# Kernel tuning notes

Measured on AMD Instinct MI355X. Metric: run time of the kernel, lower is better.

Reference implementation:

```python
import jax, jax.numpy as jnp
import numpy as np

B, C, H, W = 2, 64, 256, 256
K, DG, PAD = 3, 8, 1
KK = K * K
CG = C // DG


def _conv(x, w, b):
    y = jax.lax.conv_general_dilated(x, w, (1, 1), [(PAD, PAD), (PAD, PAD)],
                                     dimension_numbers=('NCHW', 'OIHW', 'NCHW'))
    return y + b[None, :, None, None]


def _bilinear_one(img, y, x):
    # img: (CG, H, W); y, x: (KK, H, W) float sampling coords; zero-padded bilinear
    y0 = jnp.floor(y)
    x0 = jnp.floor(x)
    wy = y - y0
    wx = x - x0

    def tap(yi, xi, wgt):
        valid = (yi >= 0) & (yi < H) & (xi >= 0) & (xi < W)
        yc = jnp.clip(yi, 0, H - 1).astype(jnp.int32)
        xc = jnp.clip(xi, 0, W - 1).astype(jnp.int32)
        v = img[:, yc, xc]  # (CG, KK, H, W)
        return v * (wgt * valid)[None]

    return (tap(y0, x0, (1 - wy) * (1 - wx)) +
            tap(y0, x0 + 1, (1 - wy) * wx) +
            tap(y0 + 1, x0, wy * (1 - wx)) +
            tap(y0 + 1, x0 + 1, wy * wx))


_sample = jax.vmap(jax.vmap(_bilinear_one))  # over batch, then deform group


def setup_inputs() -> dict:
    key = jax.random.key(0)
    ks = jax.random.split(key, 7)
    n_off = 2 * KK * DG
    n_msk = KK * DG
    bound = 1.0 / np.sqrt(C * K * K)  # kaiming_uniform(a=sqrt(5)) bound
    return {
        'ref': jax.random.normal(ks[0], (B, C, H, W), jnp.float32),
        'neighbour': jax.random.normal(ks[1], (B, C, H, W), jnp.float32),
        'off_w': jax.random.normal(ks[2], (n_off, 2 * C, K, K), jnp.float32) * 0.01,
        'off_b': jnp.zeros((n_off,), jnp.float32),
        'mask_w': jax.random.normal(ks[3], (n_msk, 2 * C, K, K), jnp.float32) * 0.01,
        'mask_b': jnp.zeros((n_msk,), jnp.float32),
        'weight': jax.random.uniform(ks[4], (C, C, K, K), jnp.float32, -bound, bound),
        'bias': jnp.zeros((C,), jnp.float32),
    }


def reference(ref, neighbour, off_w, off_b, mask_w, mask_b, weight, bias):
    concat = jnp.concatenate([ref, neighbour], axis=1)            # (B, 2C, H, W)
    offset = _conv(concat, off_w, off_b)                          # (B, 2*DG*KK, H, W)
    mask = jax.nn.sigmoid(_conv(concat, mask_w, mask_b))          # (B, DG*KK, H, W)

    off = offset.reshape(B, DG, KK, 2, H, W)
    dy, dx = off[:, :, :, 0], off[:, :, :, 1]

    ki, kj = jnp.meshgrid(jnp.arange(K), jnp.arange(K), indexing='ij')
    ki = ki.reshape(KK).astype(jnp.float32)
    kj = kj.reshape(KK).astype(jnp.float32)
    base_y = jnp.arange(H, dtype=jnp.float32)[None, :, None] - PAD + ki[:, None, None]
    base_x = jnp.arange(W, dtype=jnp.float32)[None, None, :] - PAD + kj[:, None, None]
    ys = dy + base_y                                              # (B, DG, KK, H, W)
    xs = dx + base_x

    img_g = neighbour.reshape(B, DG, CG, H, W)
    sampled = _sample(img_g, ys, xs)                              # (B, DG, CG, KK, H, W)
    sampled = sampled * mask.reshape(B, DG, 1, KK, H, W)

    wr = weight.reshape(C, DG, CG, KK)
    out = jnp.einsum('bgckhw,ogck->bohw', sampled, wr)
    return out + bias[None, :, None, None]
```

## Files before the change

### kernel.cpp

```cpp
#include <hip/hip_runtime.h>
#include <hip/hip_fp16.h>
#include <cstdint>
#include <cstddef>

#define B_ 2
#define C_ 64
#define H_ 256
#define W_ 256
#define HW_ (H_*W_)
#define DG_ 8
#define CG_ 8
#define KK_ 9
#define NOFF_ 144
#define NMSK_ 72
#define NTOT_ 216
#define KRED_ 1152
#define XPH_ 258

typedef __bf16 bf16x8 __attribute__((ext_vector_type(8)));
typedef _Float16 half8 __attribute__((ext_vector_type(8)));
typedef short  short8 __attribute__((ext_vector_type(8)));
typedef float  f32x4  __attribute__((ext_vector_type(4)));

__device__ __forceinline__ short f2bf(float f) {
    union { float f; uint32_t u; } a; a.f = f;
    uint32_t u = a.u;
    uint32_t r = (u + 0x7fffu + ((u >> 16) & 1u)) >> 16;
    return (short)r;
}

typedef __attribute__((address_space(1))) const unsigned int g_u32;
typedef __attribute__((address_space(3))) unsigned int l_u32;
__device__ __forceinline__ void gl_lds16(const void* g, void* l) {
    __builtin_amdgcn_global_load_lds((g_u32*)g, (l_u32*)l, 16, 0, 0);
}

__global__ void wtrans2_kernel(const float* __restrict__ off_w,
                               const float* __restrict__ msk_w,
                               short* __restrict__ Bw) {
    int idx = blockIdx.x * 256 + threadIdx.x;
    int s    = idx >> 13;
    int rem  = idx & 8191;
    int n    = rem >> 5;
    int slot = (rem >> 3) & 3;
    int j    = rem & 7;
    int q    = slot ^ ((n >> 1) & 3);
    int c4   = s / 9;
    int tap  = s - c4 * 9;
    int ch   = c4 * 32 + q * 8 + j;
    float v = 0.f;
    if (n < NOFF_)      v = off_w[(size_t)n * KRED_ + ch * 9 + tap];
    else if (n < NTOT_) v = msk_w[(size_t)(n - NOFF_) * KRED_ + ch * 9 + tap];
    Bw[idx] = f2bf(v);
}

__global__ void wtrans3_kernel(const float* __restrict__ weight,
                               short* __restrict__ Bw3) {
    int idx = blockIdx.x * 256 + threadIdx.x;
    int kc   = idx >> 11;
    int rem  = idx & 2047;
    int n    = rem >> 5;
    int slot = (rem >> 3) & 3;
    int j    = rem & 7;
    int q    = slot ^ ((n >> 1) & 3);
    int k    = kc >> 1;
    int g    = ((kc & 1) << 2) + q;
    int ci   = g * 8 + j;
    union { _Float16 h; short s; } cv;
    cv.h = (_Float16)weight[((size_t)n * 64 + ci) * 9 + k];
    Bw3[idx] = cv.s;
}

__global__ void pack_xp2(const float* __restrict__ ref,
                         const float* __restrict__ nbr,
                         short* __restrict__ xp,
                         short* __restrict__ nbf) {
    const int by = blockIdx.x;
    const int b  = by / XPH_;
    const int yi = by - b * XPH_;
    const int c4 = blockIdx.y;
    const int yg = yi - 1;
    const float* base = (c4 < 2 ? ref : nbr) + ((size_t)b * 64 + (c4 & 1) * 32) * HW_;
    short* rowbase = xp + (((size_t)(b * 4 + c4) * XPH_ + yi) * XPH_) * 32;
    for (int xi = threadIdx.x; xi < XPH_; xi += 256) {
        const int xg = xi - 1;
        const bool valid = ((unsigned)yg < H_) && ((unsigned)xg < W_);
        short* dst = rowbase + (size_t)xi * 32;
        const int sig = (xi >> 1) & 3;
        #pragma unroll
        for (int q = 0; q < 4; ++q) {
            float v[8];
            if (valid) {
                const float* p = base + (size_t)(q * 8) * HW_ + (size_t)yg * W_ + xg;
                #pragma unroll
                for (int j = 0; j < 8; ++j) v[j] = p[(size_t)j * HW_];
            } else {
                #pragma unroll
                for (int j = 0; j < 8; ++j) v[j] = 0.f;
            }
            short8 o;
            #pragma unroll
            for (int j = 0; j < 8; ++j) o[j] = f2bf(v[j]);
            *reinterpret_cast<short8*>(dst + ((q ^ sig) * 8)) = o;
            if (c4 >= 2 && valid) {
                const int g = (c4 - 2) * 4 + q;
                union { half8 h8; short8 s8; } u;
                #pragma unroll
                for (int j = 0; j < 8; ++j) u.h8[j] = (_Float16)v[j];
                *reinterpret_cast<short8*>(
                    nbf + ((size_t)(b * 8 + g) * HW_ + (size_t)yg * W_ + xg) * 8) = u.s8;
            }
        }
    }
}

__global__ __launch_bounds__(512, 4) void conv_mfma(
    const short* __restrict__ xp, const short* __restrict__ Bw,
    const float* __restrict__ off_b, const float* __restrict__ msk_b,
    __half* __restrict__ off_o, __half* __restrict__ msk_o)
{
    __shared__ __align__(16) short As[2][4608];

    const int tid  = threadIdx.x;
    const int lane = tid & 63;
    const int wid  = tid >> 6;
    const int wm   = wid & 1;
    const int wn   = wid >> 1;
    const int col     = lane & 15;
    const int quad    = lane >> 4;
    const int rowbase = quad * 4;

    const int bid = blockIdx.x;
    const int wg  = (bid & 7) * 128 + (bid >> 3);
    const int m0 = wg << 7;
    const int b  = m0 >> 16;
    const int h  = (m0 >> 8) & 255;
    const int w0 = m0 & 255;

    int bOff[4];
    #pragma unroll
    for (int nt = 0; nt < 4; ++nt) {
        int n = wn * 64 + nt * 16 + col;
        bOff[nt] = (n * 4 + (quad ^ ((n >> 1) & 3))) * 8;
    }
    int pxv[4];
    #pragma unroll
    for (int mt = 0; mt < 4; ++mt) pxv[mt] = wm * 64 + mt * 16 + col;

    f32x4 acc[4][4];
    #pragma unroll
    for (int i = 0; i < 4; ++i)
        #pragma unroll
        for (int j = 0; j < 4; ++j) acc[i][j] = f32x4{0.f, 0.f, 0.f, 0.f};

    auto stageA = [&](int win, int bb) {
        const int c4s = win / 3;
        const int dys = win - c4s * 3;
        const short* sA = xp + (((size_t)(b * 4 + c4s) * XPH_ + (h + dys)) * XPH_
                                + w0) * 32;
        char* dA = (char*)&As[bb][0];
        gl_lds16(sA + (size_t)tid * 8, dA + wid * 1024);
        if (tid < 32) gl_lds16(sA + (size_t)(512 + tid) * 8, dA + 8192);
    };

    stageA(0, 0);
    __syncthreads();

    #pragma unroll 1
    for (int win = 0; win < 12; ++win) {
        const int bb = win & 1;
        if (win < 11) stageA(win + 1, bb ^ 1);
        const short* AsC = &As[bb][0];

        #pragma unroll
        for (int dx = 0; dx < 3; ++dx) {
            const int s = win * 3 + dx;
            const short* bp = Bw + ((size_t)s << 13);

            bf16x8 bv[4];
            #pragma unroll
            for (int nt = 0; nt < 4; ++nt)
                bv[nt] = *reinterpret_cast<const bf16x8*>(bp + bOff[nt]);

            bf16x8 af[4];
            #pragma unroll
            for (int mt = 0; mt < 4; ++mt) {
                const int px = pxv[mt] + dx;
                af[mt] = *reinterpret_cast<const bf16x8*>(
                    &AsC[(px * 4 + (quad ^ ((px >> 1) & 3))) * 8]);
            }

            #pragma unroll
            for (int mt = 0; mt < 4; ++mt)
                #pragma unroll
                for (int nt = 0; nt < 4; ++nt)
                    acc[mt][nt] = __builtin_amdgcn_mfma_f32_16x16x32_bf16(
                        af[mt], bv[nt], acc[mt][nt], 0, 0, 0);
        }
        __syncthreads();
    }

    #pragma unroll
    for (int mt = 0; mt < 4; ++mt) {
        const int wloc = w0 + wm * 64 + mt * 16 + rowbase;
        #pragma unroll
        for (int nt = 0; nt < 4; ++nt) {
            const int n = wn * 64 + nt * 16 + col;
            if (n >= NTOT_) continue;
            const bool is_off = (n < NOFF_);
            const float bia = is_off ? off_b[n] : msk_b[n - NOFF_];
            union { uint2 u; __half hx[4]; } pk;
            #pragma unroll
            for (int rr = 0; rr < 4; ++rr) {
                float v = acc[mt][nt][rr] + bia;
                if (!is_off) v = 1.f / (1.f + __expf(-v));
                pk.hx[rr] = __float2half(v);
            }
            __half* dst = is_off
                ? (off_o + ((size_t)(b * NOFF_ + n) * H_ + h) * W_ + wloc)
                : (msk_o + ((size_t)(b * NMSK_ + (n - NOFF_)) * H_ + h) * W_ + wloc);
            *(uint2*)dst = pk.u;
        }
    }
}

struct OffV { float dy, dx, mm; };
struct GathV { half8 c00, c01, c10, c11; float a00, a01, a10, a11; };

__global__ __launch_bounds__(512, 4) void apply_mfma(
    const short* __restrict__ nbf, const __half* __restrict__ off_o,
    const __half* __restrict__ msk_o, const short* __restrict__ Bw3,
    const float* __restrict__ bias, float* __restrict__ out)
{
    __shared__ __align__(16) short As[2][128 * 32];

    const int tid  = threadIdx.x;
    const int lane = tid & 63;
    const int wid  = tid >> 6;
    const int col  = lane & 15;
    const int quad = lane >> 4;
    const int wm   = wid & 1;
    const int wn   = wid >> 1;

    const int bid = blockIdx.x;
    const int wg  = (bid & 7) * 128 + (bid >> 3);
    const int m0  = wg << 7;
    const int b   = m0 >> 16;
    const int h   = (m0 >> 8) & 255;
    const int w0  = m0 & 255;

    const int p     = tid & 127;
    const int q     = tid >> 7;
    const int w     = w0 + p;
    const int pix   = h * W_ + w;
    const int slotW = q ^ ((p >> 1) & 3);

    auto loadOffs = [&](int kc) -> OffV {
        const int k = kc >> 1;
        const int g = ((kc & 1) << 2) + q;
        OffV o;
        o.dy = __half2float(off_o[((size_t)(b * NOFF_ + g * 18 + 2 * k)) * HW_ + pix]);
        o.dx = __half2float(off_o[((size_t)(b * NOFF_ + g * 18 + 2 * k + 1)) * HW_ + pix]);
        o.mm = __half2float(msk_o[((size_t)(b * NMSK_ + g * 9 + k)) * HW_ + pix]);
        return o;
    };

    auto issueGather = [&](int kc, OffV o) -> GathV {
        const int k  = kc >> 1;
        const int g  = ((kc & 1) << 2) + q;
        const int ky = k / 3;
        const int kx = k - ky * 3;
        float ys = (float)(h - 1 + ky) + o.dy;
        float xs = (float)(w - 1 + kx) + o.dx;
        float y0f = floorf(ys), x0f = floorf(xs);
        float wy = ys - y0f, wx = xs - x0f;
        int y0 = (int)y0f, x0 = (int)x0f;
        int y1 = y0 + 1, x1 = x0 + 1;
        int yc0 = min(max(y0, 0), H_-1), yc1 = min(max(y1, 0), H_-1);
        float wy0v = (1.f - wy) * (((unsigned)y0 < H_) ? o.mm : 0.f);
        float wy1v = wy * (((unsigned)y1 < H_) ? o.mm : 0.f);
        int xb = min(max(x0, 0), W_-2);
        float wx0v = (((unsigned)x0 < W_) ? (1.f - wx) : 0.f);
        float wx1v = (((unsigned)x1 < W_) ? wx : 0.f);
        float sx0 = (x0 == xb) ? wx0v : ((x1 == xb) ? wx1v : 0.f);
        float sx1 = (x1 == xb + 1) ? wx1v : ((x0 == xb + 1) ? wx0v : 0.f);
        GathV gv;
        gv.a00 = wy0v * sx0; gv.a01 = wy0v * sx1;
        gv.a10 = wy1v * sx0; gv.a11 = wy1v * sx1;
        const short* nb = nbf + (size_t)(b * 8 + g) * HW_ * 8;
        const short* r0 = nb + ((size_t)yc0 * W_ + xb) * 8;
        const short* r1 = nb + ((size_t)yc1 * W_ + xb) * 8;
        gv.c00 = *reinterpret_cast<const half8*>(r0);
        gv.c01 = *reinterpret_cast<const half8*>(r0 + 8);
        gv.c10 = *reinterpret_cast<const half8*>(r1);
        gv.c11 = *reinterpret_cast<const half8*>(r1 + 8);
        return gv;
    };

    auto combineWrite = [&](int kc, const GathV& gv) {
        union { half8 h8; short8 s8; } u;
        #pragma unroll
        for (int c = 0; c < CG_; ++c) {
            float v = gv.a00 * (float)gv.c00[c] + gv.a01 * (float)gv.c01[c]
                    + gv.a10 * (float)gv.c10[c] + gv.a11 * (float)gv.c11[c];
            u.h8[c] = (_Float16)v;
        }
        *reinterpret_cast<short8*>(&As[kc & 1][(p * 4 + slotW) * 8]) = u.s8;
    };

    const int nB = wn * 16 + col;
    const short* bPtr = Bw3 + ((nB * 4 + (quad ^ ((nB >> 1) & 3))) << 3);

    f32x4 acc[4];
    #pragma unroll
    for (int mt = 0; mt < 4; ++mt) acc[mt] = f32x4{0.f, 0.f, 0.f, 0.f};

    {
        OffV o0 = loadOffs(0);
        GathV g0 = issueGather(0, o0);
        combineWrite(0, g0);
    }
    OffV oA = loadOffs(1);
    GathV G = issueGather(1, oA);
    oA = loadOffs(2);
    OffV oB = loadOffs(3);
    __syncthreads();

    #pragma unroll 1
    for (int kc = 0; kc < 18; ++kc) {
        const int bb = kc & 1;
        const short* AsC = &As[bb][0];

        half8 bv = *reinterpret_cast<const half8*>(bPtr + ((size_t)kc << 11));
        half8 af[4];
        #pragma unroll
        for (int mt = 0; mt < 4; ++mt) {
            const int px = wm * 64 + mt * 16 + col;
            af[mt] = *reinterpret_cast<const half8*>(
                &AsC[(px * 4 + (quad ^ ((px >> 1) & 3))) * 8]);
        }

        if (kc + 1 < 18) combineWrite(kc + 1, G);
        if (kc + 2 < 18) G = issueGather(kc + 2, oA);
        oA = oB;
        if (kc + 4 < 18) oB = loadOffs(kc + 4);

        #pragma unroll
        for (int mt = 0; mt < 4; ++mt)
            acc[mt] = __builtin_amdgcn_mfma_f32_16x16x32_f16(af[mt], bv, acc[mt], 0, 0, 0);

        __syncthreads();
    }

    const int o = wn * 16 + col;
    const float bo = bias[o];
    float* op = out + ((size_t)b * C_ + o) * HW_ + (size_t)h * W_ + w0;
    #pragma unroll
    for (int mt = 0; mt < 4; ++mt) {
        const int px = wm * 64 + mt * 16 + quad * 4;
        float4 st = make_float4(acc[mt][0] + bo, acc[mt][1] + bo,
                                acc[mt][2] + bo, acc[mt][3] + bo);
        *(float4*)(op + px) = st;
    }
}

extern "C" void kernel_launch(void* const* d_in, const int* in_sizes, int n_in,
                              void* d_out, int out_size, void* d_ws, size_t ws_size,
                              hipStream_t stream) {
    const float* ref    = (const float*)d_in[0];
    const float* nbr    = (const float*)d_in[1];
    const float* off_w  = (const float*)d_in[2];
    const float* off_b  = (const float*)d_in[3];
    const float* msk_w  = (const float*)d_in[4];
    const float* msk_b  = (const float*)d_in[5];
    const float* weight = (const float*)d_in[6];
    const float* bias   = (const float*)d_in[7];
    float* out = (float*)d_out;

    const size_t sz_off = (size_t)B_ * NOFF_ * HW_ * 2;
    const size_t sz_msk = (size_t)B_ * NMSK_ * HW_ * 2;
    const size_t sz_Bw  = (size_t)36 * 256 * 32 * 2;
    const size_t sz_xp  = (size_t)B_ * 4 * XPH_ * XPH_ * 32 * 2
                          + 16384;
    const size_t sz_Bw3 = (size_t)18 * 64 * 32 * 2;

    char* ws = (char*)d_ws;
    __half* off_o = (__half*)ws;
    __half* msk_o = (__half*)(ws + sz_off);
    short*  Bw    = (short*)(ws + sz_off + sz_msk);
    short*  xp    = (short*)(ws + sz_off + sz_msk + sz_Bw);
    short*  Bw3   = (short*)(ws + sz_off + sz_msk + sz_Bw + sz_xp);
    short*  nbf   = (short*)(ws + sz_off + sz_msk + sz_Bw + sz_xp + sz_Bw3);

    wtrans2_kernel<<<1152, 256, 0, stream>>>(off_w, msk_w, Bw);
    wtrans3_kernel<<<144, 256, 0, stream>>>(weight, Bw3);
    pack_xp2<<<dim3(B_ * XPH_, 4), 256, 0, stream>>>(ref, nbr, xp, nbf);
    conv_mfma<<<1024, 512, 0, stream>>>(xp, Bw, off_b, msk_b, off_o, msk_o);
    apply_mfma<<<1024, 512, 0, stream>>>(nbf, off_o, msk_o, Bw3, bias, out);
}
```

Before: 265.8 us.

## Fuse offset/mask conv and deformable apply into one kernel via LDS

Merges the offset/mask convolution kernel and the deformable sampling GEMM kernel into a single kernel. Offsets and sigmoid masks for the block's 128 pixels are kept in a swizzled shared-memory buffer instead of being written to and read back from global memory. This removes the intermediate global traffic and one launch. In exchange it raises shared memory per block substantially, which can lower occupancy for the latency-bound gather phase.

```diff
diff --git a/kernel.cpp b/kernel.cpp
--- a/kernel.cpp
+++ b/kernel.cpp
@@ -114,12 +114,17 @@
     }
 }
 
-__global__ __launch_bounds__(512, 4) void conv_mfma(
+struct OffV { float dy, dx, mm; };
+struct GathV { half8 c00, c01, c10, c11; float a00, a01, a10, a11; };
+
+__global__ __launch_bounds__(512, 4) void fused_conv_apply(
     const short* __restrict__ xp, const short* __restrict__ Bw,
     const float* __restrict__ off_b, const float* __restrict__ msk_b,
-    __half* __restrict__ off_o, __half* __restrict__ msk_o)
+    const short* __restrict__ nbf, const short* __restrict__ Bw3,
+    const float* __restrict__ bias, float* __restrict__ out)
 {
-    __shared__ __align__(16) short As[2][4608];
+    __shared__ __align__(16) short AsBuf[2][4608];
+    __shared__ __align__(16) short offmsk[NTOT_ * 128];
 
     const int tid  = threadIdx.x;
     const int lane = tid & 63;
@@ -137,230 +142,206 @@
     const int h  = (m0 >> 8) & 255;
     const int w0 = m0 & 255;
 
-    int bOff[4];
-    #pragma unroll
-    for (int nt = 0; nt < 4; ++nt) {
-        int n = wn * 64 + nt * 16 + col;
-        bOff[nt] = (n * 4 + (quad ^ ((n >> 1) & 3))) * 8;
+    {
+        int bOff[4];
+        #pragma unroll
+        for (int nt = 0; nt < 4; ++nt) {
+            int n = wn * 64 + nt * 16 + col;
+            bOff[nt] = (n * 4 + (quad ^ ((n >> 1) & 3))) * 8;
+        }
+        int pxv[4];
+        #pragma unroll
+        for (int mt = 0; mt < 4; ++mt) pxv[mt] = wm * 64 + mt * 16 + col;
+
+        f32x4 acc[4][4];
+        #pragma unroll
+        for (int i = 0; i < 4; ++i)
+            #pragma unroll
+            for (int j = 0; j < 4; ++j) acc[i][j] = f32x4{0.f, 0.f, 0.f, 0.f};
+
+        auto stageA = [&](int win, int bb) {
+            const int c4s = win / 3;
+            const int dys = win - c4s * 3;
+            const short* sA = xp + (((size_t)(b * 4 + c4s) * XPH_ + (h + dys)) * XPH_
+                                    + w0) * 32;
+            char* dA = (char*)&AsBuf[bb][0];
+            gl_lds16(sA + (size_t)tid * 8, dA + wid * 1024);
+            if (tid < 32) gl_lds16(sA + (size_t)(512 + tid) * 8, dA + 8192);
+        };
+
+        stageA(0, 0);
+        __syncthreads();
+
+        #pragma unroll 1
+        for (int win = 0; win < 12; ++win) {
+            const int bb = win & 1;
+            if (win < 11) stageA(win + 1, bb ^ 1);
+            const short* AsC = &AsBuf[bb][0];
+
+            #pragma unroll
+            for (int dx = 0; dx < 3; ++dx) {
+                const int s = win * 3 + dx;
+                const short* bp = Bw + ((size_t)s << 13);
+
+                bf16x8 bv[4];
+                #pragma unroll
+                for (int nt = 0; nt < 4; ++nt)
+                    bv[nt] = *reinterpret_cast<const bf16x8*>(bp + bOff[nt]);
+
+                bf16x8 af[4];
+                #pragma unroll
+                for (int mt = 0; mt < 4; ++mt) {
+                    const int px = pxv[mt] + dx;
+                    af[mt] = *reinterpret_cast<const bf16x8*>(
+                        &AsC[(px * 4 + (quad ^ ((px >> 1) & 3))) * 8]);
+                }
+
+                #pragma unroll
+                for (int mt = 0; mt < 4; ++mt)
+                    #pragma unroll
+                    for (int nt = 0; nt < 4; ++nt)
+                        acc[mt][nt] = __builtin_amdgcn_mfma_f32_16x16x32_bf16(
+                            af[mt], bv[nt], acc[mt][nt], 0, 0, 0);
+            }
+            __syncthreads();
+        }
+
+        #pragma unroll
+        for (int mt = 0; mt < 4; ++mt) {
+            const int p4 = wm * 64 + mt * 16 + rowbase;
+            #pragma unroll
+            for (int nt = 0; nt < 4; ++nt) {
+                const int n = wn * 64 + nt * 16 + col;
+                if (n >= NTOT_) continue;
+                const bool is_off = (n < NOFF_);
+                const float bia = is_off ? off_b[n] : msk_b[n - NOFF_];
+                union { uint2 u; __half hx[4]; } pk;
+                #pragma unroll
+                for (int rr = 0; rr < 4; ++rr) {
+                    float v = acc[mt][nt][rr] + bia;
+                    if (!is_off) v = 1.f / (1.f + __expf(-v));
+                    pk.hx[rr] = __float2half(v);
+                }
+                const int byt = n * 256 + ((2 * p4) ^ ((n & 7) << 4));
+                *(uint2*)((char*)offmsk + byt) = pk.u;
+            }
+        }
     }
-    int pxv[4];
-    #pragma unroll
-    for (int mt = 0; mt < 4; ++mt) pxv[mt] = wm * 64 + mt * 16 + col;
-
-    f32x4 acc[4][4];
-    #pragma unroll
-    for (int i = 0; i < 4; ++i)
-        #pragma unroll
-        for (int j = 0; j < 4; ++j) acc[i][j] = f32x4{0.f, 0.f, 0.f, 0.f};
-
-    auto stageA = [&](int win, int bb) {
-        const int c4s = win / 3;
-        const int dys = win - c4s * 3;
-        const short* sA = xp + (((size_t)(b * 4 + c4s) * XPH_ + (h + dys)) * XPH_
-                                + w0) * 32;
-        char* dA = (char*)&As[bb][0];
-        gl_lds16(sA + (size_t)tid * 8, dA + wid * 1024);
-        if (tid < 32) gl_lds16(sA + (size_t)(512 + tid) * 8, dA + 8192);
-    };
-
-    stageA(0, 0);
     __syncthreads();
 
-    #pragma unroll 1
-    for (int win = 0; win < 12; ++win) {
-        const int bb = win & 1;
-        if (win < 11) stageA(win + 1, bb ^ 1);
-        const short* AsC = &As[bb][0];
-
-        #pragma unroll
-        for (int dx = 0; dx < 3; ++dx) {
-            const int s = win * 3 + dx;
-            const short* bp = Bw + ((size_t)s << 13);
-
-            bf16x8 bv[4];
-            #pragma unroll
-            for (int nt = 0; nt < 4; ++nt)
-                bv[nt] = *reinterpret_cast<const bf16x8*>(bp + bOff[nt]);
-
-            bf16x8 af[4];
+    {
+        const int p     = tid & 127;
+        const int q     = tid >> 7;
+        const int w     = w0 + p;
+        const int slotW = q ^ ((p >> 1) & 3);
+
+        auto ldsOff = [&](int n, int pp) -> float {
+            const int byt = n * 256 + ((2 * pp) ^ ((n & 7) << 4));
+            return __half2float(*reinterpret_cast<const __half*>(
+                (const char*)offmsk + byt));
+        };
+        auto loadOffs = [&](int kc) -> OffV {
+            const int k = kc >> 1;
+            const int g = ((kc & 1) << 2) + q;
+            OffV o;
+            o.dy = ldsOff(g * 18 + 2 * k,     p);
+            o.dx = ldsOff(g * 18 + 2 * k + 1, p);
+            o.mm = ldsOff(NOFF_ + g * 9 + k,  p);
+            return o;
+        };
+
+        auto issueGather = [&](int kc, OffV o) -> GathV {
+            const int k  = kc >> 1;
+            const int g  = ((kc & 1) << 2) + q;
+            const int ky = k / 3;
+            const int kx = k - ky * 3;
+            float ys = (float)(h - 1 + ky) + o.dy;
+            float xs = (float)(w - 1 + kx) + o.dx;
+            float y0f = floorf(ys), x0f = floorf(xs);
+            float wy = ys - y0f, wx = xs - x0f;
+            int y0 = (int)y0f, x0 = (int)x0f;
+            int y1 = y0 + 1, x1 = x0 + 1;
+            int yc0 = min(max(y0, 0), H_-1), yc1 = min(max(y1, 0), H_-1);
+            float wy0v = (1.f - wy) * (((unsigned)y0 < H_) ? o.mm : 0.f);
+            float wy1v = wy * (((unsigned)y1 < H_) ? o.mm : 0.f);
+            int xb = min(max(x0, 0), W_-2);
+            float wx0v = (((unsigned)x0 < W_) ? (1.f - wx) : 0.f);
+            float wx1v = (((unsigned)x1 < W_) ? wx : 0.f);
+            float sx0 = (x0 == xb) ? wx0v : ((x1 == xb) ? wx1v : 0.f);
+            float sx1 = (x1 == xb + 1) ? wx1v : ((x0 == xb + 1) ? wx0v : 0.f);
+            GathV gv;
+            gv.a00 = wy0v * sx0; gv.a01 = wy0v * sx1;
+            gv.a10 = wy1v * sx0; gv.a11 = wy1v * sx1;
+            const short* nb = nbf + (size_t)(b * 8 + g) * HW_ * 8;
+            const short* r0 = nb + ((size_t)yc0 * W_ + xb) * 8;
+            const short* r1 = nb + ((size_t)yc1 * W_ + xb) * 8;
+            gv.c00 = *reinterpret_cast<const half8*>(r0);
+            gv.c01 = *reinterpret_cast<const half8*>(r0 + 8);
+            gv.c10 = *reinterpret_cast<const half8*>(r1);
+            gv.c11 = *reinterpret_cast<const half8*>(r1 + 8);
+            return gv;
+        };
+
+        auto combineWrite = [&](int kc, const GathV& gv) {
+            union { half8 h8; short8 s8; } u;
+            #pragma unroll
+            for (int c = 0; c < CG_; ++c) {
+                float v = gv.a00 * (float)gv.c00[c] + gv.a01 * (float)gv.c01[c]
+                        + gv.a10 * (float)gv.c10[c] + gv.a11 * (float)gv.c11[c];
+                u.h8[c] = (_Float16)v;
+            }
+            *reinterpret_cast<short8*>(&AsBuf[kc & 1][(p * 4 + slotW) * 8]) = u.s8;
+        };
+
+        const int nB = wn * 16 + col;
+        const short* bPtr = Bw3 + ((nB * 4 + (quad ^ ((nB >> 1) & 3))) << 3);
+
+        f32x4 acc2[4];
+        #pragma unroll
+        for (int mt = 0; mt < 4; ++mt) acc2[mt] = f32x4{0.f, 0.f, 0.f, 0.f};
+
+        {
+            OffV o0 = loadOffs(0);
+            GathV g0 = issueGather(0, o0);
+            combineWrite(0, g0);
+        }
+        GathV G = issueGather(1, loadOffs(1));
+        __syncthreads();
+
+        #pragma unroll 1
+        for (int kc = 0; kc < 18; ++kc) {
+            const int bb = kc & 1;
+            const short* AsC = &AsBuf[bb][0];
+
+            half8 bv = *reinterpret_cast<const half8*>(bPtr + ((size_t)kc << 11));
+            half8 af[4];
             #pragma unroll
             for (int mt = 0; mt < 4; ++mt) {
-                const int px = pxv[mt] + dx;
-                af[mt] = *reinterpret_cast<const bf16x8*>(
+                const int px = wm * 64 + mt * 16 + col;
+                af[mt] = *reinterpret_cast<const half8*>(
                     &AsC[(px * 4 + (quad ^ ((px >> 1) & 3))) * 8]);
             }
 
+            if (kc + 1 < 18) combineWrite(kc + 1, G);
+            if (kc + 2 < 18) G = issueGather(kc + 2, loadOffs(kc + 2));
+
             #pragma unroll
             for (int mt = 0; mt < 4; ++mt)
-                #pragma unroll
-                for (int nt = 0; nt < 4; ++nt)
-                    acc[mt][nt] = __builtin_amdgcn_mfma_f32_16x16x32_bf16(
-                        af[mt], bv[nt], acc[mt][nt], 0, 0, 0);
-        }
-        __syncthreads();
-    }
-
-    #pragma unroll
-    for (int mt = 0; mt < 4; ++mt) {
-        const int wloc = w0 + wm * 64 + mt * 16 + rowbase;
-        #pragma unroll
-        for (int nt = 0; nt < 4; ++nt) {
-            const int n = wn * 64 + nt * 16 + col;
-            if (n >= NTOT_) continue;
-            const bool is_off = (n < NOFF_);
-            const float bia = is_off ? off_b[n] : msk_b[n - NOFF_];
-            union { uint2 u; __half hx[4]; } pk;
-            #pragma unroll
-            for (int rr = 0; rr < 4; ++rr) {
-                float v = acc[mt][nt][rr] + bia;
-                if (!is_off) v = 1.f / (1.f + __expf(-v));
-                pk.hx[rr] = __float2half(v);
-            }
-            __half* dst = is_off
-                ? (off_o + ((size_t)(b * NOFF_ + n) * H_ + h) * W_ + wloc)
-                : (msk_o + ((size_t)(b * NMSK_ + (n - NOFF_)) * H_ + h) * W_ + wloc);
-            *(uint2*)dst = pk.u;
-        }
-    }
-}
-
-struct OffV { float dy, dx, mm; };
-struct GathV { half8 c00, c01, c10, c11; float a00, a01, a10, a11; };
-
-__global__ __launch_bounds__(512, 4) void apply_mfma(
-    const short* __restrict__ nbf, const __half* __restrict__ off_o,
-    const __half* __restrict__ msk_o, const short* __restrict__ Bw3,
-    const float* __restrict__ bias, float* __restrict__ out)
-{
-    __shared__ __align__(16) short As[2][128 * 32];
-
-    const int tid  = threadIdx.x;
-    const int lane = tid & 63;
-    const int wid  = tid >> 6;
-    const int col  = lane & 15;
-    const int quad = lane >> 4;
-    const int wm   = wid & 1;
-    const int wn   = wid >> 1;
-
-    const int bid = blockIdx.x;
-    const int wg  = (bid & 7) * 128 + (bid >> 3);
-    const int m0  = wg << 7;
-    const int b   = m0 >> 16;
-    const int h   = (m0 >> 8) & 255;
-    const int w0  = m0 & 255;
-
-    const int p     = tid & 127;
-    const int q     = tid >> 7;
-    const int w     = w0 + p;
-    const int pix   = h * W_ + w;
-    const int slotW = q ^ ((p >> 1) & 3);
-
-    auto loadOffs = [&](int kc) -> OffV {
-        const int k = kc >> 1;
-        const int g = ((kc & 1) << 2) + q;
-        OffV o;
-        o.dy = __half2float(off_o[((size_t)(b * NOFF_ + g * 18 + 2 * k)) * HW_ + pix]);
-        o.dx = __half2float(off_o[((size_t)(b * NOFF_ + g * 18 + 2 * k + 1)) * HW_ + pix]);
-        o.mm = __half2float(msk_o[((size_t)(b * NMSK_ + g * 9 + k)) * HW_ + pix]);
-        return o;
-    };
-
-    auto issueGather = [&](int kc, OffV o) -> GathV {
-        const int k  = kc >> 1;
-        const int g  = ((kc & 1) << 2) + q;
-        const int ky = k / 3;
-        const int kx = k - ky * 3;
-        float ys = (float)(h - 1 + ky) + o.dy;
-        float xs = (float)(w - 1 + kx) + o.dx;
-        float y0f = floorf(ys), x0f = floorf(xs);
-        float wy = ys - y0f, wx = xs - x0f;
-        int y0 = (int)y0f, x0 = (int)x0f;
-        int y1 = y0 + 1, x1 = x0 + 1;
-        int yc0 = min(max(y0, 0), H_-1), yc1 = min(max(y1, 0), H_-1);
-        float wy0v = (1.f - wy) * (((unsigned)y0 < H_) ? o.mm : 0.f);
-        float wy1v = wy * (((unsigned)y1 < H_) ? o.mm : 0.f);
-        int xb = min(max(x0, 0), W_-2);
-        float wx0v = (((unsigned)x0 < W_) ? (1.f - wx) : 0.f);
-        float wx1v = (((unsigned)x1 < W_) ? wx : 0.f);
-        float sx0 = (x0 == xb) ? wx0v : ((x1 == xb) ? wx1v : 0.f);
-        float sx1 = (x1 == xb + 1) ? wx1v : ((x0 == xb + 1) ? wx0v : 0.f);
-        GathV gv;
-        gv.a00 = wy0v * sx0; gv.a01 = wy0v * sx1;
-        gv.a10 = wy1v * sx0; gv.a11 = wy1v * sx1;
-        const short* nb = nbf + (size_t)(b * 8 + g) * HW_ * 8;
-        const short* r0 = nb + ((size_t)yc0 * W_ + xb) * 8;
-        const short* r1 = nb + ((size_t)yc1 * W_ + xb) * 8;
-        gv.c00 = *reinterpret_cast<const half8*>(r0);
-        gv.c01 = *reinterpret_cast<const half8*>(r0 + 8);
-        gv.c10 = *reinterpret_cast<const half8*>(r1);
-        gv.c11 = *reinterpret_cast<const half8*>(r1 + 8);
-        return gv;
-    };
-
-    auto combineWrite = [&](int kc, const GathV& gv) {
-        union { half8 h8; short8 s8; } u;
-        #pragma unroll
-        for (int c = 0; c < CG_; ++c) {
-            float v = gv.a00 * (float)gv.c00[c] + gv.a01 * (float)gv.c01[c]
-                    + gv.a10 * (float)gv.c10[c] + gv.a11 * (float)gv.c11[c];
-            u.h8[c] = (_Float16)v;
-        }
-        *reinterpret_cast<short8*>(&As[kc & 1][(p * 4 + slotW) * 8]) = u.s8;
-    };
-
-    const int nB = wn * 16 + col;
-    const short* bPtr = Bw3 + ((nB * 4 + (quad ^ ((nB >> 1) & 3))) << 3);
-
-    f32x4 acc[4];
-    #pragma unroll
-    for (int mt = 0; mt < 4; ++mt) acc[mt] = f32x4{0.f, 0.f, 0.f, 0.f};
-
-    {
-        OffV o0 = loadOffs(0);
-        GathV g0 = issueGather(0, o0);
-        combineWrite(0, g0);
-    }
-    OffV oA = loadOffs(1);
-    GathV G = issueGather(1, oA);
-    oA = loadOffs(2);
-    OffV oB = loadOffs(3);
-    __syncthreads();
-
-    #pragma unroll 1
-    for (int kc = 0; kc < 18; ++kc) {
-        const int bb = kc & 1;
-        const short* AsC = &As[bb][0];
-
-        half8 bv = *reinterpret_cast<const half8*>(bPtr + ((size_t)kc << 11));
-        half8 af[4];
+                acc2[mt] = __builtin_amdgcn_mfma_f32_16x16x32_f16(af[mt], bv, acc2[mt], 0, 0, 0);
+
+            __syncthreads();
+        }
+
+        const int o = wn * 16 + col;
+        const float bo = bias[o];
+        float* op = out + ((size_t)b * C_ + o) * HW_ + (size_t)h * W_ + w0;
         #pragma unroll
         for (int mt = 0; mt < 4; ++mt) {
-            const int px = wm * 64 + mt * 16 + col;
-            af[mt] = *reinterpret_cast<const half8*>(
-                &AsC[(px * 4 + (quad ^ ((px >> 1) & 3))) * 8]);
-        }
-
-        if (kc + 1 < 18) combineWrite(kc + 1, G);
-        if (kc + 2 < 18) G = issueGather(kc + 2, oA);
-        oA = oB;
-        if (kc + 4 < 18) oB = loadOffs(kc + 4);
-
-        #pragma unroll
-        for (int mt = 0; mt < 4; ++mt)
-            acc[mt] = __builtin_amdgcn_mfma_f32_16x16x32_f16(af[mt], bv, acc[mt], 0, 0, 0);
-
-        __syncthreads();
-    }
-
-    const int o = wn * 16 + col;
-    const float bo = bias[o];
-    float* op = out + ((size_t)b * C_ + o) * HW_ + (size_t)h * W_ + w0;
-    #pragma unroll
-    for (int mt = 0; mt < 4; ++mt) {
-        const int px = wm * 64 + mt * 16 + quad * 4;
-        float4 st = make_float4(acc[mt][0] + bo, acc[mt][1] + bo,
-                                acc[mt][2] + bo, acc[mt][3] + bo);
-        *(float4*)(op + px) = st;
+            const int px = wm * 64 + mt * 16 + quad * 4;
+            float4 st = make_float4(acc2[mt][0] + bo, acc2[mt][1] + bo,
+                                    acc2[mt][2] + bo, acc2[mt][3] + bo);
+            *(float4*)(op + px) = st;
+        }
     }
 }
 
@@ -377,24 +358,20 @@
     const float* bias   = (const float*)d_in[7];
     float* out = (float*)d_out;
 
-    const size_t sz_off = (size_t)B_ * NOFF_ * HW_ * 2;
-    const size_t sz_msk = (size_t)B_ * NMSK_ * HW_ * 2;
     const size_t sz_Bw  = (size_t)36 * 256 * 32 * 2;
     const size_t sz_xp  = (size_t)B_ * 4 * XPH_ * XPH_ * 32 * 2
                           + 16384;
     const size_t sz_Bw3 = (size_t)18 * 64 * 32 * 2;
 
     char* ws = (char*)d_ws;
-    __half* off_o = (__half*)ws;
-    __half* msk_o = (__half*)(ws + sz_off);
-    short*  Bw    = (short*)(ws + sz_off + sz_msk);
-    short*  xp    = (short*)(ws + sz_off + sz_msk + sz_Bw);
-    short*  Bw3   = (short*)(ws + sz_off + sz_msk + sz_Bw + sz_xp);
-    short*  nbf   = (short*)(ws + sz_off + sz_msk + sz_Bw + sz_xp + sz_Bw3);
+    short* Bw  = (short*)ws;
+    short* xp  = (short*)(ws + sz_Bw);
+    short* Bw3 = (short*)(ws + sz_Bw + sz_xp);
+    short* nbf = (short*)(ws + sz_Bw + sz_xp + sz_Bw3);
 
     wtrans2_kernel<<<1152, 256, 0, stream>>>(off_w, msk_w, Bw);
     wtrans3_kernel<<<144, 256, 0, stream>>>(weight, Bw3);
     pack_xp2<<<dim3(B_ * XPH_, 4), 256, 0, stream>>>(ref, nbr, xp, nbf);
-    conv_mfma<<<1024, 512, 0, stream>>>(xp, Bw, off_b, msk_b, off_o, msk_o);
-    apply_mfma<<<1024, 512, 0, stream>>>(nbf, off_o, msk_o, Bw3, bias, out);
-}
+    fused_conv_apply<<<1024, 512, 0, stream>>>(xp, Bw, off_b, msk_b,
+                                               nbf, Bw3, bias, out);
+}
```

After: 252.9 us. 1.05x faster.
